# Kernel tuning notes

Measured on AMD Instinct MI355X. Metric: run time of the kernel, lower is better.

The kernel has to match this reference:

```python
import jax, jax.numpy as jnp
import numpy as np

N_EMBD = 768
BLOCK_SIZE = 2048
ATTN_SPAN = 128
LN_EPS = 1e-5


def _band_mask(T, span):
    # mask[i, j] = 1 iff 0 <= i - j < span  (causal sliding window incl. diagonal)
    i = jnp.arange(T)[:, None]
    j = jnp.arange(T)[None, :]
    d = i - j
    return ((d >= 0) & (d < span)).astype(jnp.float32)


def setup_inputs() -> dict:
    key = jax.random.key(0)
    k1, k2, k3 = jax.random.split(key, 3)
    B, T, D = 8, BLOCK_SIZE, N_EMBD
    x = jax.random.normal(k1, (B, T, D), dtype=jnp.float32)
    W_qkv = jax.random.normal(k2, (D, 3 * D), dtype=jnp.float32) * (1.0 / np.sqrt(D))
    b_qkv = jax.random.normal(k3, (3 * D,), dtype=jnp.float32) * 0.02
    ln_w = jnp.ones((D,), dtype=jnp.float32)
    ln_b = jnp.zeros((D,), dtype=jnp.float32)
    return {"x": x, "W_qkv": W_qkv, "b_qkv": b_qkv, "ln_w": ln_w, "ln_b": ln_b}


def _layer_norm(h, w, b):
    mu = jnp.mean(h, axis=-1, keepdims=True)
    var = jnp.mean(jnp.square(h - mu), axis=-1, keepdims=True)
    return (h - mu) * jax.lax.rsqrt(var + LN_EPS) * w + b


def reference(x, W_qkv, b_qkv, ln_w, ln_b):
    B, T, D = x.shape
    qkv = x @ W_qkv + b_qkv                      # [B, T, 3D]
    q, k, v = jnp.split(qkv, 3, axis=-1)         # each [B, T, D]
    scale = jnp.float32(1.0 / np.sqrt(N_EMBD * ATTN_SPAN))
    scores = jnp.einsum('bid,bjd->bij', q, k) * scale   # [B, T, T]
    mask = _band_mask(T, ATTN_SPAN)              # [T, T]
    scores = scores * mask                       # zero outside sliding window
    out = jnp.einsum('bij,bjd->bid', scores, v)  # [B, T, D]
    return _layer_norm(out, ln_w, ln_b)
```

## Files before the change

kernel.cpp:

```cpp
#include <hip/hip_runtime.h>
#include <cstdint>
#include <cstddef>

typedef __attribute__((ext_vector_type(8))) short bf16x8;
typedef __attribute__((ext_vector_type(4))) float f32x4;
typedef __attribute__((ext_vector_type(8))) unsigned short u16x8;
typedef __attribute__((ext_vector_type(4))) unsigned short u16x4;

#define NB 8
#define NT 2048
#define ND 768
#define NC 2304
#define NM (NB*NT)
#define SPAN 128

__device__ __forceinline__ unsigned short f2bf(float f) {
    unsigned int u = __builtin_bit_cast(unsigned int, f);
    u += 0x7fffu + ((u >> 16) & 1u);
    return (unsigned short)(u >> 16);
}

#define GLOAD16(G, L) __builtin_amdgcn_global_load_lds( \
    (const __attribute__((address_space(1))) unsigned int*)(G), \
    (__attribute__((address_space(3))) unsigned int*)(L), 16, 0, 0)

__global__ void k_conv_x(const float* __restrict__ x, unsigned short* __restrict__ xb) {
    int i = blockIdx.x * 256 + threadIdx.x;
    const float4* p = (const float4*)x + (size_t)i * 2;
    float4 a = p[0], b = p[1];
    u16x8 v;
    v[0] = f2bf(a.x); v[1] = f2bf(a.y); v[2] = f2bf(a.z); v[3] = f2bf(a.w);
    v[4] = f2bf(b.x); v[5] = f2bf(b.y); v[6] = f2bf(b.z); v[7] = f2bf(b.w);
    *((u16x8*)xb + i) = v;
}

__global__ void k_conv_wT(const float* __restrict__ W, unsigned short* __restrict__ wT) {
    __shared__ unsigned short tile[64][72];
    const int k0 = blockIdx.x * 64, n0 = blockIdx.y * 64;
    const int tid = threadIdx.x;
    for (int e = 0; e < 16; ++e) {
        int idx = e * 256 + tid;
        int r = idx >> 6, c = idx & 63;
        tile[r][c] = f2bf(W[(size_t)(k0 + r) * NC + n0 + c]);
    }
    __syncthreads();
    for (int e = 0; e < 16; ++e) {
        int idx = e * 256 + tid;
        int r = idx & 63, c = idx >> 6;
        wT[(size_t)(n0 + c) * ND + k0 + r] = tile[r][c];
    }
}

__global__ __launch_bounds__(512, 2) void k_gemm(const unsigned short* __restrict__ xb,
                       const unsigned short* __restrict__ wT,
                       const float* __restrict__ bq,
                       unsigned short* __restrict__ qb,
                       unsigned short* __restrict__ kb,
                       unsigned short* __restrict__ vT) {
    __shared__ char lds[131072];
    const int tid = threadIdx.x, lane = tid & 63, w = tid >> 6;
    const int bid = blockIdx.x;
    const int mb = (bid & 7) * 8 + ((bid >> 3) & 7);
    const int nb = bid >> 6;
    const int m0 = mb * 256, n0 = nb * 256;
    const int wr = (w >> 2) * 128, wc = (w & 3) * 64;

    auto stageA = [&](int t, int h) {
        char* dst = lds + (t & 1) * 32768 + h * 16384 + w * 2048;
        const unsigned short* sb = xb + (size_t)(m0 + h * 128) * ND + t * 64;
#pragma unroll
        for (int e = 0; e < 2; ++e) {
            int s = w * 128 + e * 64 + lane;
            int r = s >> 3, sl = s & 7;
            GLOAD16(sb + (size_t)r * ND + 8 * (sl ^ (r & 7)), dst + e * 1024);
        }
    };
    auto stageB = [&](int t, int h) {
        char* dst = lds + 65536 + (t & 1) * 32768 + h * 16384 + w * 2048;
        const unsigned short* sb = wT + (size_t)(n0 + h * 128) * ND + t * 64;
#pragma unroll
        for (int e = 0; e < 2; ++e) {
            int s = w * 128 + e * 64 + lane;
            int r = s >> 3, sl = s & 7;
            GLOAD16(sb + (size_t)r * ND + 8 * (sl ^ (r & 7)), dst + e * 1024);
        }
    };

    f32x4 acc[2][4][4];
    const f32x4 zf = {0.f, 0.f, 0.f, 0.f};
#pragma unroll
    for (int s = 0; s < 2; ++s)
#pragma unroll
        for (int mi = 0; mi < 4; ++mi)
#pragma unroll
            for (int ni = 0; ni < 4; ++ni) acc[s][mi][ni] = zf;

    const int rA = wr + (lane & 15);
    const int rB = wc + (lane & 15);
    const int g16 = (lane >> 4) * 16;
    const int swA = (rA & 7) << 4, swB = (rB & 7) << 4;

    stageB(0, 0); stageB(0, 1); stageA(0, 0); stageA(0, 1);
    stageB(1, 0); stageB(1, 1);
    asm volatile("s_waitcnt vmcnt(4)" ::: "memory");
    __builtin_amdgcn_s_barrier();

#pragma unroll 1
    for (int q = 0; q < 12; ++q) {
        const char* Ab = lds + (q & 1) * 32768;
        const char* Bb = lds + 65536 + (q & 1) * 32768;
        bf16x8 Af[4], Ag[4], Bf0[4], Bf1[4];

        if (q + 1 < 12) stageA(q + 1, 0);
#pragma unroll
        for (int mi = 0; mi < 4; ++mi)
            Af[mi] = *(const bf16x8*)(Ab + (size_t)(rA + mi * 16) * 128 + (g16 ^ swA));
#pragma unroll
        for (int ni = 0; ni < 4; ++ni)
            Bf0[ni] = *(const bf16x8*)(Bb + (size_t)(rB + ni * 16) * 128 + (g16 ^ swB));
        __builtin_amdgcn_s_barrier();
        asm volatile("s_waitcnt lgkmcnt(0)" ::: "memory");
        __builtin_amdgcn_sched_barrier(0);
        __builtin_amdgcn_s_setprio(1);
#pragma unroll
        for (int mi = 0; mi < 4; ++mi)
#pragma unroll
            for (int ni = 0; ni < 4; ++ni)
                acc[0][mi][ni] = __builtin_amdgcn_mfma_f32_16x16x32_bf16(Af[mi], Bf0[ni], acc[0][mi][ni], 0, 0, 0);
        __builtin_amdgcn_s_setprio(0);
        __builtin_amdgcn_s_barrier();

        if (q + 1 < 12) stageA(q + 1, 1);
#pragma unroll
        for (int mi = 0; mi < 4; ++mi)
            Ag[mi] = *(const bf16x8*)(Ab + (size_t)(rA + 64 + mi * 16) * 128 + (g16 ^ swA));
#pragma unroll
        for (int ni = 0; ni < 4; ++ni)
            Bf1[ni] = *(const bf16x8*)(Bb + (size_t)(rB + ni * 16) * 128 + ((64 + g16) ^ swB));
        __builtin_amdgcn_s_barrier();
        asm volatile("s_waitcnt lgkmcnt(0)" ::: "memory");
        __builtin_amdgcn_sched_barrier(0);
        __builtin_amdgcn_s_setprio(1);
#pragma unroll
        for (int mi = 0; mi < 4; ++mi)
#pragma unroll
            for (int ni = 0; ni < 4; ++ni)
                acc[1][mi][ni] = __builtin_amdgcn_mfma_f32_16x16x32_bf16(Ag[mi], Bf0[ni], acc[1][mi][ni], 0, 0, 0);
        __builtin_amdgcn_s_setprio(0);
        __builtin_amdgcn_s_barrier();

        if (q + 2 < 12) stageB(q + 2, 0);
#pragma unroll
        for (int mi = 0; mi < 4; ++mi)
            Af[mi] = *(const bf16x8*)(Ab + (size_t)(rA + mi * 16) * 128 + ((64 + g16) ^ swA));
        __builtin_amdgcn_s_barrier();
        asm volatile("s_waitcnt lgkmcnt(0)" ::: "memory");
        __builtin_amdgcn_sched_barrier(0);
        __builtin_amdgcn_s_setprio(1);
#pragma unroll
        for (int mi = 0; mi < 4; ++mi)
#pragma unroll
            for (int ni = 0; ni < 4; ++ni)
                acc[0][mi][ni] = __builtin_amdgcn_mfma_f32_16x16x32_bf16(Af[mi], Bf1[ni], acc[0][mi][ni], 0, 0, 0);
        __builtin_amdgcn_s_setprio(0);
        __builtin_amdgcn_s_barrier();

        if (q + 2 < 12) stageB(q + 2, 1);
#pragma unroll
        for (int mi = 0; mi < 4; ++mi)
            Ag[mi] = *(const bf16x8*)(Ab + (size_t)(rA + 64 + mi * 16) * 128 + ((64 + g16) ^ swA));
        __builtin_amdgcn_s_barrier();
        asm volatile("s_waitcnt lgkmcnt(0)" ::: "memory");
        __builtin_amdgcn_sched_barrier(0);
        __builtin_amdgcn_s_setprio(1);
#pragma unroll
        for (int mi = 0; mi < 4; ++mi)
#pragma unroll
            for (int ni = 0; ni < 4; ++ni)
                acc[1][mi][ni] = __builtin_amdgcn_mfma_f32_16x16x32_bf16(Ag[mi], Bf1[ni], acc[1][mi][ni], 0, 0, 0);
        __builtin_amdgcn_s_setprio(0);
        if (q < 10) { asm volatile("s_waitcnt vmcnt(4)" ::: "memory"); }
        else if (q == 10) { asm volatile("s_waitcnt vmcnt(0)" ::: "memory"); }
        __builtin_amdgcn_s_barrier();
    }

    const int third = nb / 3;
    const int nl0 = (nb % 3) * 256 + wc;
    if (third < 2) {
        unsigned short* ob = third == 0 ? qb : kb;
        float bias[4];
#pragma unroll
        for (int ni = 0; ni < 4; ++ni) bias[ni] = bq[third * ND + nl0 + ni * 16 + (lane & 15)];
#pragma unroll
        for (int s = 0; s < 2; ++s)
#pragma unroll
            for (int mi = 0; mi < 4; ++mi)
#pragma unroll
                for (int e = 0; e < 4; ++e) {
                    int m = m0 + wr + (s * 4 + mi) * 16 + (lane >> 4) * 4 + e;
#pragma unroll
                    for (int ni = 0; ni < 4; ++ni)
                        ob[(size_t)m * ND + nl0 + ni * 16 + (lane & 15)] = f2bf(acc[s][mi][ni][e] + bias[ni]);
                }
    } else {
        const int bb = m0 >> 11, t0g = m0 & 2047;
        unsigned short* vTb = vT + ((size_t)bb * ND + (nb - 6) * 256) * NT;
        float bias[4];
#pragma unroll
        for (int ni = 0; ni < 4; ++ni) bias[ni] = bq[2 * ND + (nb - 6) * 256 + wc + ni * 16 + (lane & 15)];
        unsigned short* T = (unsigned short*)lds;
        for (int c = 0; c < 4; ++c) {
            __builtin_amdgcn_s_barrier();
            if ((w & 3) == c) {
#pragma unroll
                for (int s = 0; s < 2; ++s)
#pragma unroll
                    for (int mi = 0; mi < 4; ++mi)
#pragma unroll
                        for (int ni = 0; ni < 4; ++ni) {
                            int d_loc = ni * 16 + (lane & 15);
                            int t_loc = wr + (s * 4 + mi) * 16 + (lane >> 4) * 4;
                            u16x4 pk;
#pragma unroll
                            for (int e = 0; e < 4; ++e) pk[e] = f2bf(acc[s][mi][ni][e] + bias[ni]);
                            *(u16x4*)(T + d_loc * 264 + t_loc) = pk;
                        }
            }
            __builtin_amdgcn_s_barrier();
#pragma unroll
            for (int e2 = 0; e2 < 4; ++e2) {
                int slot = e2 * 512 + tid;
                int dd = slot >> 5, tc = (slot & 31) * 8;
                u16x8 v = *(const u16x8*)(T + dd * 264 + tc);
                *(u16x8*)(vTb + (size_t)(c * 64 + dd) * NT + t0g + tc) = v;
            }
        }
    }
}

__global__ __launch_bounds__(1024) void k_attn(const unsigned short* __restrict__ qb,
                       const unsigned short* __restrict__ kb,
                       const unsigned short* __restrict__ vT,
                       const float* __restrict__ lnw,
                       const float* __restrict__ lnb,
                       float* __restrict__ out) {
    __shared__ char smem[123904];
    unsigned short* S = (unsigned short*)smem;
    char* R = smem + 25600;

    const int tid = threadIdx.x, lane = tid & 63, w = tid >> 6;
    const int bid = blockIdx.x;
    const int nid = (bid & 7) * 32 + (bid >> 3);
    const int b = nid >> 5;
    const int q0 = (nid & 31) * 64;
    const size_t rowQ = (size_t)b * NT + q0;
    const size_t rowK = (size_t)b * NT;
    const size_t vbase = (size_t)b * ND * NT;

    f32x4 sacc[3];
    const f32x4 zf = {0.f, 0.f, 0.f, 0.f};
#pragma unroll
    for (int s = 0; s < 3; ++s) sacc[s] = zf;

    const int qrow = (w >> 2) * 16 + (lane & 15);
    const int kct = (w & 3) * 3;

    auto stage_qk = [&](int dc, int cur) {
        char* L = R + cur * 32768;
#pragma unroll
        for (int e = 0; e < 2; ++e) {
            int s = w * 128 + e * 64 + lane;
            const unsigned short* src;
            if (s < 512) {
                int r = s >> 3, sl = s & 7;
                src = qb + (rowQ + r) * ND + dc * 64 + 8 * (sl ^ (r & 7));
            } else {
                int t = s - 512;
                int r = t >> 3, sl = t & 7;
                int j = q0 - 128 + r; if (j < 0) j = 0;
                src = kb + (rowK + j) * ND + dc * 64 + 8 * (sl ^ (r & 7));
            }
            GLOAD16(src, L + (w * 128 + e * 64) * 16);
        }
    };

    stage_qk(0, 0);
    __syncthreads();
    for (int dc = 0; dc < 12; ++dc) {
        int cur = dc & 1;
        if (dc < 11) stage_qk(dc + 1, cur ^ 1);
        const char* Lq = R + cur * 32768;
        const char* Lk = Lq + 8192;
#pragma unroll
        for (int kk = 0; kk < 2; ++kk) {
            int bq_ = (((lane >> 4) * 16 + kk * 64)) ^ ((qrow & 7) << 4);
            bf16x8 aq = *(const bf16x8*)(Lq + qrow * 128 + bq_);
#pragma unroll
            for (int s = 0; s < 3; ++s) {
                int krow = (kct + s) * 16 + (lane & 15);
                int bk_ = (((lane >> 4) * 16 + kk * 64)) ^ ((krow & 7) << 4);
                bf16x8 bk = *(const bf16x8*)(Lk + krow * 128 + bk_);
                sacc[s] = __builtin_amdgcn_mfma_f32_16x16x32_bf16(aq, bk, sacc[s], 0, 0, 0);
            }
        }
        __syncthreads();
    }

    const float scl = 0.0031894436f;
#pragma unroll
    for (int s = 0; s < 3; ++s) {
        int jl = (kct + s) * 16 + (lane & 15);
        int j = q0 - 128 + jl;
#pragma unroll
        for (int e = 0; e < 4; ++e) {
            int il = (w >> 2) * 16 + (lane >> 4) * 4 + e;
            int d = (q0 + il) - j;
            float v = (d >= 0 && d < SPAN && j >= 0) ? sacc[s][e] * scl : 0.0f;
            S[il * 200 + jl] = f2bf(v);
        }
    }

    auto stage_v = [&](int c, int cur) {
        char* L = R + cur * 49152;
        int j0 = q0 - 128 + c * 32;
#pragma unroll
        for (int e = 0; e < 3; ++e) {
            int s = w * 192 + e * 64 + lane;
            int d = s >> 2, sl = s & 3;
            int j = j0 + 8 * (sl ^ (d & 3)); if (j < 0) j = 0;
            GLOAD16(vT + vbase + (size_t)d * NT + j, L + (w * 192 + e * 64) * 16);
        }
    };

    f32x4 acc[4][3];
#pragma unroll
    for (int rt = 0; rt < 4; ++rt)
#pragma unroll
        for (int ct = 0; ct < 3; ++ct) acc[rt][ct] = zf;

    stage_v(0, 0);
    __syncthreads();
    for (int c = 0; c < 6; ++c) {
        int cur = c & 1;
        if (c < 5) stage_v(c + 1, cur ^ 1);
        const char* Lv = R + cur * 49152;
        bf16x8 as[4], bv[3];
#pragma unroll
        for (int rt = 0; rt < 4; ++rt)
            as[rt] = *(const bf16x8*)((const char*)S + (rt * 16 + (lane & 15)) * 400 + c * 64 + (lane >> 4) * 16);
#pragma unroll
        for (int ct = 0; ct < 3; ++ct) {
            int d = (w * 3 + ct) * 16 + (lane & 15);
            bv[ct] = *(const bf16x8*)(Lv + d * 64 + (((lane >> 4) * 16) ^ ((d & 3) << 4)));
        }
#pragma unroll
        for (int rt = 0; rt < 4; ++rt)
#pragma unroll
            for (int ct = 0; ct < 3; ++ct)
                acc[rt][ct] = __builtin_amdgcn_mfma_f32_16x16x32_bf16(as[rt], bv[ct], acc[rt][ct], 0, 0, 0);
        __syncthreads();
    }

    float psum[4][4], pssq[4][4];
#pragma unroll
    for (int rt = 0; rt < 4; ++rt)
#pragma unroll
        for (int e = 0; e < 4; ++e) {
            float s = 0.f, q = 0.f;
#pragma unroll
            for (int ct = 0; ct < 3; ++ct) { float v = acc[rt][ct][e]; s += v; q += v * v; }
            psum[rt][e] = s; pssq[rt][e] = q;
        }
#pragma unroll
    for (int mx = 1; mx < 16; mx <<= 1)
#pragma unroll
        for (int rt = 0; rt < 4; ++rt)
#pragma unroll
            for (int e = 0; e < 4; ++e) {
                psum[rt][e] += __shfl_xor(psum[rt][e], mx, 64);
                pssq[rt][e] += __shfl_xor(pssq[rt][e], mx, 64);
            }

    float* P = (float*)R;
    float* F = (float*)(R + 8192);
    if ((lane & 15) == 0) {
#pragma unroll
        for (int rt = 0; rt < 4; ++rt)
#pragma unroll
            for (int e = 0; e < 4; ++e) {
                int r = rt * 16 + (lane >> 4) * 4 + e;
                P[(r * 16 + w) * 2] = psum[rt][e];
                P[(r * 16 + w) * 2 + 1] = pssq[rt][e];
            }
    }
    __syncthreads();
    if (tid < 64) {
        float s = 0.f, q = 0.f;
#pragma unroll
        for (int ww = 0; ww < 16; ++ww) { s += P[(tid * 16 + ww) * 2]; q += P[(tid * 16 + ww) * 2 + 1]; }
        float mu = s * (1.0f / 768.0f);
        float var = q * (1.0f / 768.0f) - mu * mu;
        F[tid * 2] = mu;
        F[tid * 2 + 1] = rsqrtf(var + 1e-5f);
    }
    __syncthreads();

    float lw[3], lb_[3];
#pragma unroll
    for (int ct = 0; ct < 3; ++ct) {
        int dcol = (w * 3 + ct) * 16 + (lane & 15);
        lw[ct] = lnw[dcol]; lb_[ct] = lnb[dcol];
    }
#pragma unroll
    for (int rt = 0; rt < 4; ++rt)
#pragma unroll
        for (int e = 0; e < 4; ++e) {
            int row = rt * 16 + (lane >> 4) * 4 + e;
            float mu = F[row * 2], rs = F[row * 2 + 1];
            float* rowp = out + (rowQ + row) * ND;
#pragma unroll
            for (int ct = 0; ct < 3; ++ct) {
                int dcol = (w * 3 + ct) * 16 + (lane & 15);
                rowp[dcol] = (acc[rt][ct][e] - mu) * rs * lw[ct] + lb_[ct];
            }
        }
}

extern "C" void kernel_launch(void* const* d_in, const int* in_sizes, int n_in,
                              void* d_out, int out_size, void* d_ws, size_t ws_size,
                              hipStream_t stream) {
    const float* x   = (const float*)d_in[0];
    const float* W   = (const float*)d_in[1];
    const float* bqv = (const float*)d_in[2];
    const float* lnw = (const float*)d_in[3];
    const float* lnb = (const float*)d_in[4];
    float* out = (float*)d_out;

    char* ws = (char*)d_ws;
    const size_t SZ_XB = (size_t)NM * ND * 2;
    const size_t SZ_WT = (size_t)NC * ND * 2;
    const size_t SZ_P  = (size_t)NM * ND * 2;
    unsigned short* xb = (unsigned short*)ws;
    unsigned short* wT = (unsigned short*)(ws + SZ_XB);
    unsigned short* qb = (unsigned short*)(ws + SZ_XB + SZ_WT);
    unsigned short* kb = (unsigned short*)(ws + SZ_XB + SZ_WT + SZ_P);
    unsigned short* vT = (unsigned short*)(ws + SZ_XB + SZ_WT + 2 * SZ_P);

    k_conv_x<<<dim3(NM * ND / (256 * 8)), dim3(256), 0, stream>>>(x, xb);
    k_conv_wT<<<dim3(ND / 64, NC / 64), dim3(256), 0, stream>>>(W, wT);
    k_gemm<<<dim3(576), dim3(512), 0, stream>>>(xb, wT, bqv, qb, kb, vT);
    k_attn<<<dim3(256), dim3(1024), 0, stream>>>(qb, kb, vT, lnw, lnb, out);
}
```

Before: 130.0 us.

## Merge prep kernels, restructure GEMM k-loop fragments, relax attention barriers

The two conversion kernels become one launch, with block ranges split between the x cast and the W transpose, which removes a launch. The QKV GEMM is reorganized to load both k-halves of each fragment at once and to reuse the A and B fragments across four quadrant phases, with a changed staging lane mapping. Its launch bounds drop to one block per SM, which allows more registers. In the attention kernel, __syncthreads after the async loads is replaced by explicit vmcnt waits plus s_barrier so that prefetches overlap compute, at some risk to correctness of the synchronization.

```diff
diff --git a/kernel.cpp b/kernel.cpp
--- a/kernel.cpp
+++ b/kernel.cpp
@@ -24,34 +24,36 @@
     (const __attribute__((address_space(1))) unsigned int*)(G), \
     (__attribute__((address_space(3))) unsigned int*)(L), 16, 0, 0)
 
-__global__ void k_conv_x(const float* __restrict__ x, unsigned short* __restrict__ xb) {
-    int i = blockIdx.x * 256 + threadIdx.x;
-    const float4* p = (const float4*)x + (size_t)i * 2;
-    float4 a = p[0], b = p[1];
-    u16x8 v;
-    v[0] = f2bf(a.x); v[1] = f2bf(a.y); v[2] = f2bf(a.z); v[3] = f2bf(a.w);
-    v[4] = f2bf(b.x); v[5] = f2bf(b.y); v[6] = f2bf(b.z); v[7] = f2bf(b.w);
-    *((u16x8*)xb + i) = v;
+__global__ void k_prep(const float* __restrict__ x, unsigned short* __restrict__ xb,
+                       const float* __restrict__ W, unsigned short* __restrict__ wT) {
+    __shared__ unsigned short tile[64][72];
+    const int bid = blockIdx.x, tid = threadIdx.x;
+    if (bid < 6144) {
+        int i = bid * 256 + tid;
+        const float4* p = (const float4*)x + (size_t)i * 2;
+        float4 a = p[0], b = p[1];
+        u16x8 v;
+        v[0] = f2bf(a.x); v[1] = f2bf(a.y); v[2] = f2bf(a.z); v[3] = f2bf(a.w);
+        v[4] = f2bf(b.x); v[5] = f2bf(b.y); v[6] = f2bf(b.z); v[7] = f2bf(b.w);
+        *((u16x8*)xb + i) = v;
+    } else {
+        int b2 = bid - 6144;
+        const int k0 = (b2 % 12) * 64, n0 = (b2 / 12) * 64;
+        for (int e = 0; e < 16; ++e) {
+            int idx = e * 256 + tid;
+            int r = idx >> 6, c = idx & 63;
+            tile[r][c] = f2bf(W[(size_t)(k0 + r) * NC + n0 + c]);
+        }
+        __syncthreads();
+        for (int e = 0; e < 16; ++e) {
+            int idx = e * 256 + tid;
+            int r = idx & 63, c = idx >> 6;
+            wT[(size_t)(n0 + c) * ND + k0 + r] = tile[r][c];
+        }
+    }
 }
 
-__global__ void k_conv_wT(const float* __restrict__ W, unsigned short* __restrict__ wT) {
-    __shared__ unsigned short tile[64][72];
-    const int k0 = blockIdx.x * 64, n0 = blockIdx.y * 64;
-    const int tid = threadIdx.x;
-    for (int e = 0; e < 16; ++e) {
-        int idx = e * 256 + tid;
-        int r = idx >> 6, c = idx & 63;
-        tile[r][c] = f2bf(W[(size_t)(k0 + r) * NC + n0 + c]);
-    }
-    __syncthreads();
-    for (int e = 0; e < 16; ++e) {
-        int idx = e * 256 + tid;
-        int r = idx & 63, c = idx >> 6;
-        wT[(size_t)(n0 + c) * ND + k0 + r] = tile[r][c];
-    }
-}
-
-__global__ __launch_bounds__(512, 2) void k_gemm(const unsigned short* __restrict__ xb,
+__global__ __launch_bounds__(512, 1) void k_gemm(const unsigned short* __restrict__ xb,
                        const unsigned short* __restrict__ wT,
                        const float* __restrict__ bq,
                        unsigned short* __restrict__ qb,
@@ -64,175 +66,194 @@
     const int nb = bid >> 6;
     const int m0 = mb * 256, n0 = nb * 256;
     const int wr = (w >> 2) * 128, wc = (w & 3) * 64;
+    const int laneCol = lane & 15, laneK = lane >> 4;
+    const int sw = (laneCol & 7) << 4;
 
     auto stageA = [&](int t, int h) {
-        char* dst = lds + (t & 1) * 32768 + h * 16384 + w * 2048;
+        char* dst = lds + (t & 1) * 32768 + h * 16384 + w * 1024;
         const unsigned short* sb = xb + (size_t)(m0 + h * 128) * ND + t * 64;
 #pragma unroll
         for (int e = 0; e < 2; ++e) {
-            int s = w * 128 + e * 64 + lane;
+            int s = e * 512 + w * 64 + lane;
             int r = s >> 3, sl = s & 7;
-            GLOAD16(sb + (size_t)r * ND + 8 * (sl ^ (r & 7)), dst + e * 1024);
+            GLOAD16(sb + (size_t)r * ND + 8 * (sl ^ (r & 7)), dst + e * 8192);
         }
     };
     auto stageB = [&](int t, int h) {
-        char* dst = lds + 65536 + (t & 1) * 32768 + h * 16384 + w * 2048;
+        char* dst = lds + 65536 + (t & 1) * 32768 + h * 16384 + w * 1024;
         const unsigned short* sb = wT + (size_t)(n0 + h * 128) * ND + t * 64;
 #pragma unroll
         for (int e = 0; e < 2; ++e) {
-            int s = w * 128 + e * 64 + lane;
+            int s = e * 512 + w * 64 + lane;
             int r = s >> 3, sl = s & 7;
-            GLOAD16(sb + (size_t)r * ND + 8 * (sl ^ (r & 7)), dst + e * 1024);
+            GLOAD16(sb + (size_t)r * ND + 8 * (sl ^ (r & 7)), dst + e * 8192);
         }
     };
 
-    f32x4 acc[2][4][4];
+    f32x4 acc[2][2][4][2];
     const f32x4 zf = {0.f, 0.f, 0.f, 0.f};
 #pragma unroll
-    for (int s = 0; s < 2; ++s)
-#pragma unroll
-        for (int mi = 0; mi < 4; ++mi)
-#pragma unroll
-            for (int ni = 0; ni < 4; ++ni) acc[s][mi][ni] = zf;
-
-    const int rA = wr + (lane & 15);
-    const int rB = wc + (lane & 15);
-    const int g16 = (lane >> 4) * 16;
-    const int swA = (rA & 7) << 4, swB = (rB & 7) << 4;
-
-    stageB(0, 0); stageB(0, 1); stageA(0, 0); stageA(0, 1);
+    for (int a = 0; a < 2; ++a)
+#pragma unroll
+        for (int b = 0; b < 2; ++b)
+#pragma unroll
+            for (int c = 0; c < 4; ++c)
+#pragma unroll
+                for (int d = 0; d < 2; ++d) acc[a][b][c][d] = zf;
+
+    stageA(0, 0); stageA(0, 1); stageB(0, 0); stageB(0, 1);
     stageB(1, 0); stageB(1, 1);
     asm volatile("s_waitcnt vmcnt(4)" ::: "memory");
     __builtin_amdgcn_s_barrier();
 
+    bf16x8 Af[4][2], B0[2][2], B1[2][2];
 #pragma unroll 1
-    for (int q = 0; q < 12; ++q) {
-        const char* Ab = lds + (q & 1) * 32768;
-        const char* Bb = lds + 65536 + (q & 1) * 32768;
-        bf16x8 Af[4], Ag[4], Bf0[4], Bf1[4];
-
-        if (q + 1 < 12) stageA(q + 1, 0);
-#pragma unroll
-        for (int mi = 0; mi < 4; ++mi)
-            Af[mi] = *(const bf16x8*)(Ab + (size_t)(rA + mi * 16) * 128 + (g16 ^ swA));
-#pragma unroll
-        for (int ni = 0; ni < 4; ++ni)
-            Bf0[ni] = *(const bf16x8*)(Bb + (size_t)(rB + ni * 16) * 128 + (g16 ^ swB));
+    for (int t = 0; t < 12; ++t) {
+        const char* Ab = lds + (t & 1) * 32768;
+        const char* Bb = lds + 65536 + (t & 1) * 32768;
+
+#pragma unroll
+        for (int mi = 0; mi < 4; ++mi)
+#pragma unroll
+            for (int kk = 0; kk < 2; ++kk)
+                Af[mi][kk] = *(const bf16x8*)(Ab + (size_t)(wr + mi * 16 + laneCol) * 128 +
+                                              ((kk * 64 + laneK * 16) ^ sw));
+#pragma unroll
+        for (int ci = 0; ci < 2; ++ci)
+#pragma unroll
+            for (int kk = 0; kk < 2; ++kk)
+                B0[ci][kk] = *(const bf16x8*)(Bb + (size_t)(wc + ci * 16 + laneCol) * 128 +
+                                              ((kk * 64 + laneK * 16) ^ sw));
+        if (t + 1 < 12) stageA(t + 1, 0);
         __builtin_amdgcn_s_barrier();
         asm volatile("s_waitcnt lgkmcnt(0)" ::: "memory");
-        __builtin_amdgcn_sched_barrier(0);
         __builtin_amdgcn_s_setprio(1);
 #pragma unroll
         for (int mi = 0; mi < 4; ++mi)
 #pragma unroll
-            for (int ni = 0; ni < 4; ++ni)
-                acc[0][mi][ni] = __builtin_amdgcn_mfma_f32_16x16x32_bf16(Af[mi], Bf0[ni], acc[0][mi][ni], 0, 0, 0);
+            for (int ci = 0; ci < 2; ++ci)
+#pragma unroll
+                for (int kk = 0; kk < 2; ++kk)
+                    acc[0][0][mi][ci] = __builtin_amdgcn_mfma_f32_16x16x32_bf16(Af[mi][kk], B0[ci][kk], acc[0][0][mi][ci], 0, 0, 0);
         __builtin_amdgcn_s_setprio(0);
         __builtin_amdgcn_s_barrier();
 
-        if (q + 1 < 12) stageA(q + 1, 1);
-#pragma unroll
-        for (int mi = 0; mi < 4; ++mi)
-            Ag[mi] = *(const bf16x8*)(Ab + (size_t)(rA + 64 + mi * 16) * 128 + (g16 ^ swA));
-#pragma unroll
-        for (int ni = 0; ni < 4; ++ni)
-            Bf1[ni] = *(const bf16x8*)(Bb + (size_t)(rB + ni * 16) * 128 + ((64 + g16) ^ swB));
+#pragma unroll
+        for (int ci = 0; ci < 2; ++ci)
+#pragma unroll
+            for (int kk = 0; kk < 2; ++kk)
+                B1[ci][kk] = *(const bf16x8*)(Bb + (size_t)(wc + 32 + ci * 16 + laneCol) * 128 +
+                                              ((kk * 64 + laneK * 16) ^ sw));
+        if (t + 1 < 12) stageA(t + 1, 1);
         __builtin_amdgcn_s_barrier();
         asm volatile("s_waitcnt lgkmcnt(0)" ::: "memory");
-        __builtin_amdgcn_sched_barrier(0);
         __builtin_amdgcn_s_setprio(1);
 #pragma unroll
         for (int mi = 0; mi < 4; ++mi)
 #pragma unroll
-            for (int ni = 0; ni < 4; ++ni)
-                acc[1][mi][ni] = __builtin_amdgcn_mfma_f32_16x16x32_bf16(Ag[mi], Bf0[ni], acc[1][mi][ni], 0, 0, 0);
+            for (int ci = 0; ci < 2; ++ci)
+#pragma unroll
+                for (int kk = 0; kk < 2; ++kk)
+                    acc[0][1][mi][ci] = __builtin_amdgcn_mfma_f32_16x16x32_bf16(Af[mi][kk], B1[ci][kk], acc[0][1][mi][ci], 0, 0, 0);
         __builtin_amdgcn_s_setprio(0);
         __builtin_amdgcn_s_barrier();
 
-        if (q + 2 < 12) stageB(q + 2, 0);
-#pragma unroll
-        for (int mi = 0; mi < 4; ++mi)
-            Af[mi] = *(const bf16x8*)(Ab + (size_t)(rA + mi * 16) * 128 + ((64 + g16) ^ swA));
+#pragma unroll
+        for (int mi = 0; mi < 4; ++mi)
+#pragma unroll
+            for (int kk = 0; kk < 2; ++kk)
+                Af[mi][kk] = *(const bf16x8*)(Ab + (size_t)(wr + 64 + mi * 16 + laneCol) * 128 +
+                                              ((kk * 64 + laneK * 16) ^ sw));
+        if (t + 2 < 12) stageB(t + 2, 0);
         __builtin_amdgcn_s_barrier();
         asm volatile("s_waitcnt lgkmcnt(0)" ::: "memory");
-        __builtin_amdgcn_sched_barrier(0);
         __builtin_amdgcn_s_setprio(1);
 #pragma unroll
         for (int mi = 0; mi < 4; ++mi)
 #pragma unroll
-            for (int ni = 0; ni < 4; ++ni)
-                acc[0][mi][ni] = __builtin_amdgcn_mfma_f32_16x16x32_bf16(Af[mi], Bf1[ni], acc[0][mi][ni], 0, 0, 0);
+            for (int ci = 0; ci < 2; ++ci)
+#pragma unroll
+                for (int kk = 0; kk < 2; ++kk)
+                    acc[1][0][mi][ci] = __builtin_amdgcn_mfma_f32_16x16x32_bf16(Af[mi][kk], B0[ci][kk], acc[1][0][mi][ci], 0, 0, 0);
         __builtin_amdgcn_s_setprio(0);
         __builtin_amdgcn_s_barrier();
 
-        if (q + 2 < 12) stageB(q + 2, 1);
-#pragma unroll
-        for (int mi = 0; mi < 4; ++mi)
-            Ag[mi] = *(const bf16x8*)(Ab + (size_t)(rA + 64 + mi * 16) * 128 + ((64 + g16) ^ swA));
-        __builtin_amdgcn_s_barrier();
-        asm volatile("s_waitcnt lgkmcnt(0)" ::: "memory");
-        __builtin_amdgcn_sched_barrier(0);
+        if (t + 2 < 12) stageB(t + 2, 1);
+        if (t < 10) { asm volatile("s_waitcnt vmcnt(4)" ::: "memory"); }
+        else if (t == 10) { asm volatile("s_waitcnt vmcnt(0)" ::: "memory"); }
+        __builtin_amdgcn_s_barrier();
         __builtin_amdgcn_s_setprio(1);
 #pragma unroll
         for (int mi = 0; mi < 4; ++mi)
 #pragma unroll
-            for (int ni = 0; ni < 4; ++ni)
-                acc[1][mi][ni] = __builtin_amdgcn_mfma_f32_16x16x32_bf16(Ag[mi], Bf1[ni], acc[1][mi][ni], 0, 0, 0);
+            for (int ci = 0; ci < 2; ++ci)
+#pragma unroll
+                for (int kk = 0; kk < 2; ++kk)
+                    acc[1][1][mi][ci] = __builtin_amdgcn_mfma_f32_16x16x32_bf16(Af[mi][kk], B1[ci][kk], acc[1][1][mi][ci], 0, 0, 0);
         __builtin_amdgcn_s_setprio(0);
-        if (q < 10) { asm volatile("s_waitcnt vmcnt(4)" ::: "memory"); }
-        else if (q == 10) { asm volatile("s_waitcnt vmcnt(0)" ::: "memory"); }
         __builtin_amdgcn_s_barrier();
     }
 
     const int third = nb / 3;
-    const int nl0 = (nb % 3) * 256 + wc;
+    const int np = (nb % 3) * 256;
     if (third < 2) {
         unsigned short* ob = third == 0 ? qb : kb;
-        float bias[4];
-#pragma unroll
-        for (int ni = 0; ni < 4; ++ni) bias[ni] = bq[third * ND + nl0 + ni * 16 + (lane & 15)];
-#pragma unroll
-        for (int s = 0; s < 2; ++s)
+        float bias[2][2];
+#pragma unroll
+        for (int nh = 0; nh < 2; ++nh)
+#pragma unroll
+            for (int ci = 0; ci < 2; ++ci)
+                bias[nh][ci] = bq[third * ND + np + wc + nh * 32 + ci * 16 + laneCol];
+#pragma unroll
+        for (int mh = 0; mh < 2; ++mh)
 #pragma unroll
             for (int mi = 0; mi < 4; ++mi)
 #pragma unroll
                 for (int e = 0; e < 4; ++e) {
-                    int m = m0 + wr + (s * 4 + mi) * 16 + (lane >> 4) * 4 + e;
-#pragma unroll
-                    for (int ni = 0; ni < 4; ++ni)
-                        ob[(size_t)m * ND + nl0 + ni * 16 + (lane & 15)] = f2bf(acc[s][mi][ni][e] + bias[ni]);
+                    int m = m0 + wr + mh * 64 + mi * 16 + laneK * 4 + e;
+#pragma unroll
+                    for (int nh = 0; nh < 2; ++nh)
+#pragma unroll
+                        for (int ci = 0; ci < 2; ++ci)
+                            ob[(size_t)m * ND + np + wc + nh * 32 + ci * 16 + laneCol]
+                                = f2bf(acc[mh][nh][mi][ci][e] + bias[nh][ci]);
                 }
     } else {
         const int bb = m0 >> 11, t0g = m0 & 2047;
-        unsigned short* vTb = vT + ((size_t)bb * ND + (nb - 6) * 256) * NT;
-        float bias[4];
-#pragma unroll
-        for (int ni = 0; ni < 4; ++ni) bias[ni] = bq[2 * ND + (nb - 6) * 256 + wc + ni * 16 + (lane & 15)];
+        unsigned short* vTb = vT + ((size_t)bb * ND + np) * NT;
+        float bias[2][2];
+#pragma unroll
+        for (int nh = 0; nh < 2; ++nh)
+#pragma unroll
+            for (int ci = 0; ci < 2; ++ci)
+                bias[nh][ci] = bq[2 * ND + np + wc + nh * 32 + ci * 16 + laneCol];
         unsigned short* T = (unsigned short*)lds;
         for (int c = 0; c < 4; ++c) {
             __builtin_amdgcn_s_barrier();
             if ((w & 3) == c) {
 #pragma unroll
-                for (int s = 0; s < 2; ++s)
+                for (int mh = 0; mh < 2; ++mh)
 #pragma unroll
                     for (int mi = 0; mi < 4; ++mi)
 #pragma unroll
-                        for (int ni = 0; ni < 4; ++ni) {
-                            int d_loc = ni * 16 + (lane & 15);
-                            int t_loc = wr + (s * 4 + mi) * 16 + (lane >> 4) * 4;
-                            u16x4 pk;
-#pragma unroll
-                            for (int e = 0; e < 4; ++e) pk[e] = f2bf(acc[s][mi][ni][e] + bias[ni]);
-                            *(u16x4*)(T + d_loc * 264 + t_loc) = pk;
-                        }
+                        for (int nh = 0; nh < 2; ++nh)
+#pragma unroll
+                            for (int ci = 0; ci < 2; ++ci) {
+                                int d_loc = nh * 32 + ci * 16 + laneCol;
+                                int t_loc = wr + mh * 64 + mi * 16 + laneK * 4;
+                                u16x4 pk;
+#pragma unroll
+                                for (int e = 0; e < 4; ++e) pk[e] = f2bf(acc[mh][nh][mi][ci][e] + bias[nh][ci]);
+                                *(u16x4*)(T + d_loc * 264 + t_loc) = pk;
+                            }
             }
             __builtin_amdgcn_s_barrier();
 #pragma unroll
             for (int e2 = 0; e2 < 4; ++e2) {
                 int slot = e2 * 512 + tid;
-                int dd = slot >> 5, tc = (slot & 31) * 8;
-                u16x8 v = *(const u16x8*)(T + dd * 264 + tc);
-                *(u16x8*)(vTb + (size_t)(c * 64 + dd) * NT + t0g + tc) = v;
+                int dd = slot >> 5, ch = slot & 31;
+                u16x8 v = *(const u16x8*)(T + dd * 264 + ch * 8);
+                *(u16x8*)(vTb + (size_t)(c * 64 + dd) * NT + t0g + ch * 8) = v;
             }
         }
     }
@@ -285,10 +306,15 @@
     };
 
     stage_qk(0, 0);
-    __syncthreads();
     for (int dc = 0; dc < 12; ++dc) {
         int cur = dc & 1;
-        if (dc < 11) stage_qk(dc + 1, cur ^ 1);
+        if (dc < 11) {
+            stage_qk(dc + 1, cur ^ 1);
+            asm volatile("s_waitcnt vmcnt(2)" ::: "memory");
+        } else {
+            asm volatile("s_waitcnt vmcnt(0)" ::: "memory");
+        }
+        __builtin_amdgcn_s_barrier();
         const char* Lq = R + cur * 32768;
         const char* Lk = Lq + 8192;
 #pragma unroll
@@ -303,7 +329,7 @@
                 sacc[s] = __builtin_amdgcn_mfma_f32_16x16x32_bf16(aq, bk, sacc[s], 0, 0, 0);
             }
         }
-        __syncthreads();
+        __builtin_amdgcn_s_barrier();
     }
 
     const float scl = 0.0031894436f;
@@ -319,6 +345,7 @@
             S[il * 200 + jl] = f2bf(v);
         }
     }
+    asm volatile("s_waitcnt lgkmcnt(0)" ::: "memory");
 
     auto stage_v = [&](int c, int cur) {
         char* L = R + cur * 49152;
@@ -339,10 +366,15 @@
         for (int ct = 0; ct < 3; ++ct) acc[rt][ct] = zf;
 
     stage_v(0, 0);
-    __syncthreads();
     for (int c = 0; c < 6; ++c) {
         int cur = c & 1;
-        if (c < 5) stage_v(c + 1, cur ^ 1);
+        if (c < 5) {
+            stage_v(c + 1, cur ^ 1);
+            asm volatile("s_waitcnt vmcnt(3)" ::: "memory");
+        } else {
+            asm volatile("s_waitcnt vmcnt(0)" ::: "memory");
+        }
+        __builtin_amdgcn_s_barrier();
         const char* Lv = R + cur * 49152;
         bf16x8 as[4], bv[3];
 #pragma unroll
@@ -358,7 +390,7 @@
 #pragma unroll
             for (int ct = 0; ct < 3; ++ct)
                 acc[rt][ct] = __builtin_amdgcn_mfma_f32_16x16x32_bf16(as[rt], bv[ct], acc[rt][ct], 0, 0, 0);
-        __syncthreads();
+        __builtin_amdgcn_s_barrier();
     }
 
     float psum[4][4], pssq[4][4];
@@ -446,8 +478,7 @@
     unsigned short* kb = (unsigned short*)(ws + SZ_XB + SZ_WT + SZ_P);
     unsigned short* vT = (unsigned short*)(ws + SZ_XB + SZ_WT + 2 * SZ_P);
 
-    k_conv_x<<<dim3(NM * ND / (256 * 8)), dim3(256), 0, stream>>>(x, xb);
-    k_conv_wT<<<dim3(ND / 64, NC / 64), dim3(256), 0, stream>>>(W, wT);
+    k_prep<<<dim3(6576), dim3(256), 0, stream>>>(x, xb, W, wT);
     k_gemm<<<dim3(576), dim3(512), 0, stream>>>(xb, wT, bqv, qb, kb, vT);
     k_attn<<<dim3(256), dim3(1024), 0, stream>>>(qb, kb, vT, lnw, lnb, out);
 }
```

New measurement: 126.2 us. -2.9%, faster.
